# Performance work log

Hardware: AMD Instinct MI355X
Metric: run time of the kernel (lower is better)

Reference implementation:

```python
import jax, jax.numpy as jnp
import numpy as np

B, C, H, W = 4, 256, 128, 128
HEADS = 8
EPS_LN = 1e-5
EPS_NORM = 1e-12


def conv2d(x, w, padding, groups=1):
    return jax.lax.conv_general_dilated(
        x, w, window_strides=(1, 1), padding=padding,
        feature_group_count=groups,
        dimension_numbers=('NCHW', 'OIHW', 'NCHW'))


def layernorm_c(x, weight, bias):
    # WithBias LayerNorm over channel dim (to_3d makes channels the last axis)
    mu = jnp.mean(x, axis=1, keepdims=True)
    var = jnp.var(x, axis=1, keepdims=True)
    xn = (x - mu) / jnp.sqrt(var + EPS_LN)
    return xn * weight[None, :, None, None] + bias[None, :, None, None]


def setup_inputs() -> dict:
    key = jax.random.key(0)
    ks = jax.random.split(key, 8)
    s = 0.02
    return {
        'x': jax.random.normal(ks[0], (B, C, H, W), jnp.float32),
        'y': jax.random.normal(ks[1], (B, C, H, W), jnp.float32),
        'ln_kv_w': jnp.ones((C,), jnp.float32),
        'ln_kv_b': jnp.zeros((C,), jnp.float32),
        'ln_q_w': jnp.ones((C,), jnp.float32),
        'ln_q_b': jnp.zeros((C,), jnp.float32),
        'W_kv': jax.random.normal(ks[2], (2 * C, C, 1, 1), jnp.float32) * s,
        'W_dw': jax.random.normal(ks[3], (2 * C, 1, 3, 3), jnp.float32) * s,
        'W_q': jax.random.normal(ks[4], (C, C, 3, 3), jnp.float32) * s,
        'W_proj': jax.random.normal(ks[5], (C, C, 1, 1), jnp.float32) * s,
        'temperature': jnp.ones((HEADS, 1, 1), jnp.float32),
    }


def reference(x, y, ln_kv_w, ln_kv_b, ln_q_w, ln_q_b, W_kv, W_dw, W_q, W_proj, temperature):
    b, c, h, w = x.shape
    xn = layernorm_c(x, ln_kv_w, ln_kv_b)
    yn = layernorm_c(y, ln_q_w, ln_q_b)

    # Attention (MDTA channel cross-attention)
    kv = conv2d(xn, W_kv, 'VALID')                       # [b, 2c, h, w]
    kv = conv2d(kv, W_dw, 'SAME', groups=2 * c)          # depthwise 3x3
    k, v = jnp.split(kv, 2, axis=1)
    q = conv2d(yn, W_q, 'SAME')                          # [b, c, h, w]

    def heads(t):
        return t.reshape(b, HEADS, c // HEADS, h * w)    # [b, head, ch, hw]

    q, k, v = heads(q), heads(k), heads(v)
    q = q / jnp.maximum(jnp.linalg.norm(q, axis=-1, keepdims=True), EPS_NORM)
    k = k / jnp.maximum(jnp.linalg.norm(k, axis=-1, keepdims=True), EPS_NORM)

    attn = jnp.einsum('bhcn,bhdn->bhcd', q, k) * temperature[None]
    attn = jax.nn.softmax(attn, axis=-1)
    out = jnp.einsum('bhcd,bhdn->bhcn', attn, v)         # [b, head, ch, hw]
    out = out.reshape(b, c, h, w)
    out = conv2d(out, W_proj, 'VALID')
    return yn + out
```

## Files before the change

kernel.cpp:

```cpp
#include <hip/hip_runtime.h>
#include <hip/hip_bf16.h>

typedef __hip_bfloat16 bf16;
typedef __attribute__((ext_vector_type(8))) short bf16x8;
typedef __attribute__((ext_vector_type(4))) float f32x4;

#define Bn 4
#define Cn 256
#define C2n 512
#define Hn 128
#define Wn 128
#define HWn 16384
#define HEADSn 8
#define CHn 32
#define PADW 132
#define PADH 130
#define PROW (PADW * Cn)
#define PBn ((size_t)PADH * PROW)

static __device__ __forceinline__ float b2f(bf16 v) { return __bfloat162float(v); }
static __device__ __forceinline__ bf16 f2b(float v) { return __float2bfloat16(v); }
static __device__ __forceinline__ short f2bs(float v) {
    bf16 t = f2b(v);
    return __builtin_bit_cast(short, t);
}
static __device__ __forceinline__ float s2f(short s) {
    bf16 t = __builtin_bit_cast(bf16, s);
    return b2f(t);
}

static __device__ __forceinline__ void gload16(const void* g, void* l) {
    __builtin_amdgcn_global_load_lds(
        (const __attribute__((address_space(1))) unsigned int*)g,
        (__attribute__((address_space(3))) unsigned int*)l,
        16, 0, 0);
}


__global__ void cast_kernel(const float* __restrict__ src, bf16* __restrict__ dst, int n) {
    for (int i = blockIdx.x * 256 + threadIdx.x; i < n; i += gridDim.x * 256)
        dst[i] = f2b(src[i]);
}

__global__ void wq_repack_kernel(const float* __restrict__ Wq, bf16* __restrict__ wr) {
    int i = blockIdx.x * 256 + threadIdx.x;
    if (i < Cn * Cn) {
        int oc = i >> 8, c = i & 255;
        #pragma unroll
        for (int dy = 0; dy < 3; dy++)
            #pragma unroll
            for (int dx = 0; dx < 3; dx++)
                wr[((size_t)dy * Cn + oc) * 768 + dx * Cn + c] =
                    f2b(Wq[(size_t)i * 9 + dy * 3 + dx]);
    }
}

__global__ void halo_zero_kernel(bf16* __restrict__ yp) {
    int yq = blockIdx.x;
    int b  = blockIdx.y;
    bf16* row = yp + (size_t)b * PBn + (size_t)yq * PROW;
    bf16x8 z = {0, 0, 0, 0, 0, 0, 0, 0};
    if (yq == 0 || yq == PADH - 1) {
        for (int i = threadIdx.x; i < PROW / 8; i += 256)
            *(bf16x8*)&row[(size_t)i * 8] = z;
    } else {
        for (int i = threadIdx.x; i < 128; i += 256) {
            if (i < 32) *(bf16x8*)&row[(size_t)i * 8] = z;
            else        *(bf16x8*)&row[(size_t)129 * Cn + (size_t)(i - 32) * 8] = z;
        }
    }
}

__global__ void ln_kernel(const float* __restrict__ x,
                          const float* __restrict__ gw,
                          const float* __restrict__ gb,
                          bf16* __restrict__ o16) {
    __shared__ float sw[Cn], sb[Cn];
    int tid = threadIdx.x;
    if (tid < Cn) { sw[tid] = gw[tid]; sb[tid] = gb[tid]; }
    __syncthreads();
    int pix = blockIdx.x * 256 + tid;
    int b = pix >> 14;
    int hw = pix & (HWn - 1);
    const float* xb = x + (size_t)b * Cn * HWn + hw;
    float s = 0.f, ss = 0.f;
    for (int c = 0; c < Cn; c++) {
        float v = xb[(size_t)c * HWn];
        s += v; ss += v * v;
    }
    float mu  = s * (1.f / Cn);
    float var = ss * (1.f / Cn) - mu * mu;
    float inv = rsqrtf(var + 1e-5f);
    bf16* ob = o16 + (size_t)b * Cn * HWn + hw;
    for (int c = 0; c < Cn; c++) {
        float v = (xb[(size_t)c * HWn] - mu) * inv * sw[c] + sb[c];
        ob[(size_t)c * HWn] = f2b(v);
    }
}

__global__ void transpose_kernel(const bf16* __restrict__ src, bf16* __restrict__ dst) {
    __shared__ unsigned int t[64][65];
    int tid = threadIdx.x;
    int pxt = blockIdx.x;
    int ct  = blockIdx.y;
    int b   = blockIdx.z;
    const bf16* sb = src + ((size_t)b * Cn + ct * 64) * HWn + pxt * 64;
    for (int i = tid; i < 512; i += 256) {
        int r = i >> 3, sg = (i & 7) * 8;
        bf16x8 v = *(const bf16x8*)&sb[(size_t)r * HWn + sg];
        #pragma unroll
        for (int j = 0; j < 8; j++) t[r][sg + j] = (unsigned int)(unsigned short)v[j];
    }
    __syncthreads();
    bf16* db = dst + ((size_t)b * HWn + pxt * 64) * Cn + ct * 64;
    for (int i = tid; i < 512; i += 256) {
        int r = i >> 3, sg = (i & 7) * 8;
        bf16x8 v;
        #pragma unroll
        for (int j = 0; j < 8; j++) v[j] = (short)(unsigned short)t[sg + j][r];
        *(bf16x8*)&db[(size_t)r * Cn + sg] = v;
    }
}

__global__ void transpose_pad_kernel(const bf16* __restrict__ src, bf16* __restrict__ dst) {
    __shared__ unsigned int t[64][65];
    int tid = threadIdx.x;
    int pxt = blockIdx.x;
    int ct  = blockIdx.y;
    int b   = blockIdx.z;
    const bf16* sb = src + ((size_t)b * Cn + ct * 64) * HWn + pxt * 64;
    for (int i = tid; i < 512; i += 256) {
        int r = i >> 3, sg = (i & 7) * 8;
        bf16x8 v = *(const bf16x8*)&sb[(size_t)r * HWn + sg];
        #pragma unroll
        for (int j = 0; j < 8; j++) t[r][sg + j] = (unsigned int)(unsigned short)v[j];
    }
    __syncthreads();
    int p0 = pxt * 64;
    int yr = p0 >> 7, x0 = p0 & 127;
    bf16* db = dst + (size_t)b * PBn
                   + ((size_t)(yr + 1) * PADW + (x0 + 1)) * Cn + ct * 64;
    for (int i = tid; i < 512; i += 256) {
        int r = i >> 3, sg = (i & 7) * 8;
        bf16x8 v;
        #pragma unroll
        for (int j = 0; j < 8; j++) v[j] = (short)(unsigned short)t[sg + j][r];
        *(bf16x8*)&db[(size_t)r * Cn + sg] = v;
    }
}

__global__ __launch_bounds__(256) void kv1x1_mfma_kernel(
        const bf16* __restrict__ xn_pm,
        const bf16* __restrict__ wkv_pk,
        bf16* __restrict__ kv) {
    __shared__ __attribute__((aligned(16))) short Als[8192];
    __shared__ __attribute__((aligned(16))) short Bls[8192];
    int tid  = threadIdx.x;
    int px0  = blockIdx.x * 128;
    int oc0  = blockIdx.y * 128;
    int b    = blockIdx.z;
    int wave = tid >> 6, lane = tid & 63;
    int lm = lane & 15, kq = lane >> 4;
    int l7 = lm & 7;

    f32x4 acc[2][8];
    #pragma unroll
    for (int mt = 0; mt < 2; mt++)
        #pragma unroll
        for (int nt = 0; nt < 8; nt++) acc[mt][nt] = (f32x4){0.f, 0.f, 0.f, 0.f};

    int rA = tid >> 3;
    int cA = (tid & 7) ^ (rA & 7);
    const short* pA = (const short*)wkv_pk + ((size_t)(oc0 + rA)) * Cn + cA * 8;
    const short* pB = (const short*)xn_pm + ((size_t)b * HWn + px0 + rA) * Cn + cA * 8;
    short* lA = &Als[wave * 512];
    short* lB = &Bls[wave * 512];

    for (int kc = 0; kc < Cn; kc += 64) {
        __syncthreads();
        #pragma unroll
        for (int j = 0; j < 4; j++) {
            gload16(pA + kc + j * (32 * Cn), lA + j * 2048);
            gload16(pB + kc + j * (32 * Cn), lB + j * 2048);
        }
        __syncthreads();
        #pragma unroll
        for (int kk = 0; kk < 2; kk++) {
            int xo = (((kk << 2) | kq) ^ l7) * 8;
            bf16x8 afr[2], bfr[8];
            #pragma unroll
            for (int mt = 0; mt < 2; mt++)
                afr[mt] = *(const bf16x8*)&Als[(wave * 32 + mt * 16 + lm) * 64 + xo];
            #pragma unroll
            for (int nt = 0; nt < 8; nt++)
                bfr[nt] = *(const bf16x8*)&Bls[(nt * 16 + lm) * 64 + xo];
            #pragma unroll
            for (int mt = 0; mt < 2; mt++)
                #pragma unroll
                for (int nt = 0; nt < 8; nt++)
                    acc[mt][nt] = __builtin_amdgcn_mfma_f32_16x16x32_bf16(
                        afr[mt], bfr[nt], acc[mt][nt], 0, 0, 0);
        }
    }
    bf16* kb = kv + ((size_t)b * C2n + oc0) * HWn + px0;
    #pragma unroll
    for (int mt = 0; mt < 2; mt++) {
        int ocl = wave * 32 + mt * 16 + kq * 4;
        #pragma unroll
        for (int nt = 0; nt < 8; nt++) {
            int pxx = nt * 16 + lm;
            #pragma unroll
            for (int r = 0; r < 4; r++)
                kb[(size_t)(ocl + r) * HWn + pxx] = f2b(acc[mt][nt][r]);
        }
    }
}

__global__ void dw_kernel(const bf16* __restrict__ kv,
                          const float* __restrict__ Wdw,
                          bf16* __restrict__ kvdw) {
    __shared__ float st[18][132];
    int tid = threadIdx.x;
    int r0  = blockIdx.x * 16;
    int ch  = blockIdx.y;
    int b   = blockIdx.z;
    float w[9];
    #pragma unroll
    for (int t = 0; t < 9; t++) w[t] = Wdw[ch * 9 + t];
    const bf16* base = kv + ((size_t)b * C2n + ch) * HWn;
    if (tid < 18) { st[tid][0] = 0.f; st[tid][129] = 0.f; }
    for (int i = tid; i < 288; i += 256) {
        int row = i >> 4, sg = (i & 15) << 3;
        int gr = r0 - 1 + row;
        bf16x8 v = {0, 0, 0, 0, 0, 0, 0, 0};
        if (gr >= 0 && gr < Hn) v = *(const bf16x8*)&base[(size_t)gr * Wn + sg];
        #pragma unroll
        for (int j = 0; j < 8; j++) st[row][1 + sg + j] = s2f(v[j]);
    }
    __syncthreads();
    int orow = tid >> 4, sg = (tid & 15) << 3;
    float o[8];
    #pragma unroll
    for (int j = 0; j < 8; j++) o[j] = 0.f;
    #pragma unroll
    for (int dy = 0; dy < 3; dy++)
        #pragma unroll
        for (int dx = 0; dx < 3; dx++) {
            float ww = w[dy * 3 + dx];
            #pragma unroll
            for (int j = 0; j < 8; j++) o[j] += ww * st[orow + dy][sg + j + dx];
        }
    bf16x8 ov;
    #pragma unroll
    for (int j = 0; j < 8; j++) ov[j] = f2bs(o[j]);
    *(bf16x8*)&kvdw[((size_t)b * C2n + ch) * HWn + (size_t)(r0 + orow) * Wn + sg] = ov;
}

__global__ __launch_bounds__(256) void qconv_mfma_kernel(
        const bf16* __restrict__ ypad,
        const bf16* __restrict__ wq_r,
        bf16* __restrict__ q) {
    __shared__ __attribute__((aligned(16))) short Als[8192];
    __shared__ __attribute__((aligned(16))) short Bls[8192];
    int tid  = threadIdx.x;
    int xb_  = blockIdx.x;
    int y    = ((xb_ & 7) << 4) | (xb_ >> 3);
    int oc0  = blockIdx.y * 128;
    int b    = blockIdx.z;
    int wave = tid >> 6, lane = tid & 63;
    int lm = lane & 15, kq = lane >> 4;
    int l7 = lm & 7;

    f32x4 acc[2][8];
    #pragma unroll
    for (int mt = 0; mt < 2; mt++)
        #pragma unroll
        for (int nt = 0; nt < 8; nt++) acc[mt][nt] = (f32x4){0.f, 0.f, 0.f, 0.f};

    int rA = tid >> 3;
    int cA = (tid & 7) ^ (rA & 7);
    const short* pA = (const short*)wq_r + ((size_t)(oc0 + rA)) * 768 + cA * 8;
    const short* pB = (const short*)ypad + (size_t)b * PBn + (size_t)y * PROW
                    + (size_t)rA * Cn + cA * 8;
    short* lA = &Als[wave * 512];
    short* lB = &Bls[wave * 512];

    for (int dy = 0; dy < 3; dy++) {
        const short* wd = pA + (size_t)dy * (Cn * 768);
        const short* yd = pB + (size_t)dy * PROW;
        for (int kc = 0; kc < 768; kc += 64) {
            __syncthreads();
            #pragma unroll
            for (int j = 0; j < 4; j++) {
                gload16(wd + kc + j * (32 * 768), lA + j * 2048);
                gload16(yd + kc + j * (32 * Cn), lB + j * 2048);
            }
            __syncthreads();
            #pragma unroll
            for (int kk = 0; kk < 2; kk++) {
                int xo = (((kk << 2) | kq) ^ l7) * 8;
                bf16x8 afr[2], bfr[8];
                #pragma unroll
                for (int mt = 0; mt < 2; mt++)
                    afr[mt] = *(const bf16x8*)&Als[(wave * 32 + mt * 16 + lm) * 64 + xo];
                #pragma unroll
                for (int nt = 0; nt < 8; nt++)
                    bfr[nt] = *(const bf16x8*)&Bls[(nt * 16 + lm) * 64 + xo];
                #pragma unroll
                for (int mt = 0; mt < 2; mt++)
                    #pragma unroll
                    for (int nt = 0; nt < 8; nt++)
                        acc[mt][nt] = __builtin_amdgcn_mfma_f32_16x16x32_bf16(
                            afr[mt], bfr[nt], acc[mt][nt], 0, 0, 0);
            }
        }
    }
    bf16* qb = q + ((size_t)b * Cn + oc0) * HWn + (size_t)y * Wn;
    #pragma unroll
    for (int mt = 0; mt < 2; mt++) {
        int ocl = wave * 32 + mt * 16 + kq * 4;
        #pragma unroll
        for (int nt = 0; nt < 8; nt++) {
            int px = nt * 16 + lm;
            #pragma unroll
            for (int r = 0; r < 4; r++)
                qb[(size_t)(ocl + r) * HWn + px] = f2b(acc[mt][nt][r]);
        }
    }
}

__global__ __launch_bounds__(256) void attn_qk_kernel(
        const bf16* __restrict__ q,
        const bf16* __restrict__ kvdw,
        float* __restrict__ partial,
        float* __restrict__ qkp) {
    __shared__ short qls[32 * 264];
    __shared__ short kls[32 * 264];
    __shared__ float sred[4][1024];
    int tid   = threadIdx.x;
    int split = blockIdx.x;
    int bh    = blockIdx.y;
    int b = bh >> 3, h = bh & 7;
    int wave = tid >> 6, lane = tid & 63;
    int lm = lane & 15, kq = lane >> 4;

    const short* qbase = (const short*)(q    + ((size_t)(b * Cn  + h * CHn)) * HWn) + split * 2048;
    const short* kbase = (const short*)(kvdw + ((size_t)(b * C2n + h * CHn)) * HWn) + split * 2048;

    f32x4 acc[2][2];
    #pragma unroll
    for (int mt = 0; mt < 2; mt++)
        #pragma unroll
        for (int nt = 0; nt < 2; nt++) acc[mt][nt] = (f32x4){0.f, 0.f, 0.f, 0.f};

    float qss[4] = {0.f, 0.f, 0.f, 0.f};
    float kss[4] = {0.f, 0.f, 0.f, 0.f};
    int rb = tid >> 5, sgc = (tid & 31) * 8;

    for (int n0 = 0; n0 < 2048; n0 += 256) {
        __syncthreads();
        #pragma unroll
        for (int j = 0; j < 4; j++) {
            int r = rb + j * 8;
            bf16x8 qv = *(const bf16x8*)&qbase[(size_t)r * HWn + n0 + sgc];
            bf16x8 kv = *(const bf16x8*)&kbase[(size_t)r * HWn + n0 + sgc];
            *(bf16x8*)&qls[r * 264 + sgc] = qv;
            *(bf16x8*)&kls[r * 264 + sgc] = kv;
            #pragma unroll
            for (int e = 0; e < 8; e++) {
                float qf = s2f(qv[e]), kf = s2f(kv[e]);
                qss[j] += qf * qf;
                kss[j] += kf * kf;
            }
        }
        __syncthreads();
        int nb = wave * 64;
        #pragma unroll
        for (int kk = 0; kk < 64; kk += 32) {
            bf16x8 afr[2], bfr[2];
            #pragma unroll
            for (int mt = 0; mt < 2; mt++)
                afr[mt] = *(const bf16x8*)&qls[(mt * 16 + lm) * 264 + nb + kk + kq * 8];
            #pragma unroll
            for (int nt = 0; nt < 2; nt++)
                bfr[nt] = *(const bf16x8*)&kls[(nt * 16 + lm) * 264 + nb + kk + kq * 8];
            #pragma unroll
            for (int mt = 0; mt < 2; mt++)
                #pragma unroll
                for (int nt = 0; nt < 2; nt++)
                    acc[mt][nt] = __builtin_amdgcn_mfma_f32_16x16x32_bf16(
                        afr[mt], bfr[nt], acc[mt][nt], 0, 0, 0);
        }
    }
    __syncthreads();
    #pragma unroll
    for (int mt = 0; mt < 2; mt++)
        #pragma unroll
        for (int nt = 0; nt < 2; nt++)
            #pragma unroll
            for (int r = 0; r < 4; r++) {
                int c = mt * 16 + kq * 4 + r;
                int d = nt * 16 + lm;
                sred[wave][c * 32 + d] = acc[mt][nt][r];
            }
    #pragma unroll
    for (int off = 16; off > 0; off >>= 1) {
        #pragma unroll
        for (int j = 0; j < 4; j++) {
            qss[j] += __shfl_xor(qss[j], off);
            kss[j] += __shfl_xor(kss[j], off);
        }
    }
    if ((tid & 31) == 0) {
        float* qp = qkp + ((size_t)bh * 8 + split) * 64;
        #pragma unroll
        for (int j = 0; j < 4; j++) {
            qp[rb + 8 * j]      = qss[j];
            qp[32 + rb + 8 * j] = kss[j];
        }
    }
    __syncthreads();
    float* pb = partial + ((size_t)bh * 8 + split) * 1024;
    for (int i = tid; i < 1024; i += 256)
        pb[i] = sred[0][i] + sred[1][i] + sred[2][i] + sred[3][i];
}

__global__ void attn_softmax_kernel(const float* __restrict__ partial,
                                    const float* __restrict__ qkp,
                                    const float* __restrict__ temp,
                                    float* __restrict__ attn) {
    __shared__ float S[1024];
    __shared__ float sc[64];
    int bh = blockIdx.x;
    int h = bh & 7;
    int tid = threadIdx.x;
    if (tid < 64) {
        float s = 0.f;
        #pragma unroll
        for (int sp = 0; sp < 8; sp++)
            s += qkp[((size_t)bh * 8 + sp) * 64 + tid];
        sc[tid] = 1.f / fmaxf(sqrtf(s), 1e-12f);
    }
    __syncthreads();
    for (int i = tid; i < 1024; i += 256) {
        float v = 0.f;
        #pragma unroll
        for (int sp = 0; sp < 8; sp++)
            v += partial[((size_t)bh * 8 + sp) * 1024 + i];
        int c = i >> 5, d = i & 31;
        v *= sc[c] * sc[32 + d] * temp[h];
        S[i] = v;
    }
    __syncthreads();
    if (tid < 32) {
        int c = tid;
        float m = -1e30f;
        for (int d = 0; d < 32; d++) m = fmaxf(m, S[c * 32 + d]);
        float sum = 0.f;
        for (int d = 0; d < 32; d++) sum += __expf(S[c * 32 + d] - m);
        float inv = 1.f / sum;
        for (int d = 0; d < 32; d++)
            attn[(size_t)bh * 1024 + c * 32 + d] = __expf(S[c * 32 + d] - m) * inv;
    }
}

__global__ void av_kernel(const float* __restrict__ attn,
                          const bf16* __restrict__ kvdw,
                          bf16* __restrict__ ao_pm) {
    int bh = blockIdx.y;
    int b = bh >> 3, h = bh & 7;
    int tid = threadIdx.x;
    int n = blockIdx.x * 256 + tid;
    __shared__ float At[32][32];
    for (int i = tid; i < 1024; i += 256) {
        int cc = i >> 5, dd = i & 31;
        At[dd][cc] = attn[((size_t)bh * 32 + cc) * 32 + dd];
    }
    __syncthreads();
    const bf16* vbase = kvdw + ((size_t)b * C2n + Cn + h * CHn) * HWn;
    float acc[32];
    #pragma unroll
    for (int c = 0; c < 32; c++) acc[c] = 0.f;
    for (int d = 0; d < 32; d++) {
        float vv = b2f(vbase[(size_t)d * HWn + n]);
        #pragma unroll
        for (int c = 0; c < 32; c++) acc[c] += At[d][c] * vv;
    }
    bf16* obase = ao_pm + ((size_t)b * HWn + n) * Cn + h * CHn;
    #pragma unroll
    for (int g = 0; g < 4; g++) {
        bf16x8 v;
        #pragma unroll
        for (int j = 0; j < 8; j++) v[j] = f2bs(acc[g * 8 + j]);
        *(bf16x8*)&obase[g * 8] = v;
    }
}

__global__ __launch_bounds__(256) void proj_mfma_kernel(
        const bf16* __restrict__ ao_pm,
        const bf16* __restrict__ wpr_pk,
        const bf16* __restrict__ ypad,
        float* __restrict__ out) {
    __shared__ __attribute__((aligned(16))) short Als[8192];
    __shared__ __attribute__((aligned(16))) short Bls[8192];
    int tid  = threadIdx.x;
    int y    = blockIdx.x;
    int px0  = y * 128;
    int oc0  = blockIdx.y * 128;
    int b    = blockIdx.z;
    int wave = tid >> 6, lane = tid & 63;
    int lm = lane & 15, kq = lane >> 4;
    int l7 = lm & 7;

    f32x4 acc[2][8];
    #pragma unroll
    for (int mt = 0; mt < 2; mt++)
        #pragma unroll
        for (int nt = 0; nt < 8; nt++) acc[mt][nt] = (f32x4){0.f, 0.f, 0.f, 0.f};

    int rA = tid >> 3;
    int cA = (tid & 7) ^ (rA & 7);
    const short* pA = (const short*)wpr_pk + ((size_t)(oc0 + rA)) * Cn + cA * 8;
    const short* pB = (const short*)ao_pm + ((size_t)b * HWn + px0 + rA) * Cn + cA * 8;
    short* lA = &Als[wave * 512];
    short* lB = &Bls[wave * 512];

    for (int kc = 0; kc < Cn; kc += 64) {
        __syncthreads();
        #pragma unroll
        for (int j = 0; j < 4; j++) {
            gload16(pA + kc + j * (32 * Cn), lA + j * 2048);
            gload16(pB + kc + j * (32 * Cn), lB + j * 2048);
        }
        __syncthreads();
        #pragma unroll
        for (int kk = 0; kk < 2; kk++) {
            int xo = (((kk << 2) | kq) ^ l7) * 8;
            bf16x8 afr[2], bfr[8];
            #pragma unroll
            for (int mt = 0; mt < 2; mt++)
                afr[mt] = *(const bf16x8*)&Als[(wave * 32 + mt * 16 + lm) * 64 + xo];
            #pragma unroll
            for (int nt = 0; nt < 8; nt++)
                bfr[nt] = *(const bf16x8*)&Bls[(nt * 16 + lm) * 64 + xo];
            #pragma unroll
            for (int mt = 0; mt < 2; mt++)
                #pragma unroll
                for (int nt = 0; nt < 8; nt++)
                    acc[mt][nt] = __builtin_amdgcn_mfma_f32_16x16x32_bf16(
                        afr[mt], bfr[nt], acc[mt][nt], 0, 0, 0);
        }
    }
    const short* ynp = (const short*)ypad + (size_t)b * PBn
                     + ((size_t)(y + 1) * PADW + 1) * Cn;
    float* ob = out + ((size_t)b * Cn + oc0) * HWn + px0;
    #pragma unroll
    for (int mt = 0; mt < 2; mt++) {
        int ocl = wave * 32 + mt * 16 + kq * 4;
        #pragma unroll
        for (int nt = 0; nt < 8; nt++) {
            int px = nt * 16 + lm;
            #pragma unroll
            for (int r = 0; r < 4; r++)
                ob[(size_t)(ocl + r) * HWn + px] =
                    acc[mt][nt][r] + s2f(ynp[(size_t)px * Cn + oc0 + ocl + r]);
        }
    }
}

extern "C" void kernel_launch(void* const* d_in, const int* in_sizes, int n_in,
                              void* d_out, int out_size, void* d_ws, size_t ws_size,
                              hipStream_t stream) {
    const float* x     = (const float*)d_in[0];
    const float* y     = (const float*)d_in[1];
    const float* lnkw  = (const float*)d_in[2];
    const float* lnkb  = (const float*)d_in[3];
    const float* lnqw  = (const float*)d_in[4];
    const float* lnqb  = (const float*)d_in[5];
    const float* Wkv   = (const float*)d_in[6];
    const float* Wdw   = (const float*)d_in[7];
    const float* Wq    = (const float*)d_in[8];
    const float* Wproj = (const float*)d_in[9];
    const float* temp  = (const float*)d_in[10];
    float* out = (float*)d_out;

    char* ws = (char*)d_ws;
    const size_t TENB = (size_t)Bn * Cn * HWn * 2;
    bf16* xn_cm = (bf16*)ws;
    bf16* kvb   = (bf16*)ws;
    bf16* q_cm  = (bf16*)ws;
    bf16* yn_cm = (bf16*)(ws + 2 * TENB);
    bf16* kvdw  = (bf16*)(ws + 2 * TENB);
    bf16*  xn_pm = (bf16*)(ws + 4 * TENB);
    bf16*  ao_pm = xn_pm;
    float* partS = (float*)(ws + 4 * TENB);
    bf16* yn_pad = (bf16*)(ws + 5 * TENB);
    char* wp = ws + 5 * TENB + (size_t)Bn * PBn * 2;
    bf16* wq_r   = (bf16*)wp;  wp += (size_t)3 * Cn * 768 * 2;
    bf16* wkv_pk = (bf16*)wp;  wp += (size_t)C2n * Cn * 2;
    bf16* wpr_pk = (bf16*)wp;  wp += (size_t)Cn * Cn * 2;
    float* qkp   = (float*)wp; wp += 65536;
    float* attnP = (float*)wp; wp += 131072;

    wq_repack_kernel<<<dim3(256), 256, 0, stream>>>(Wq, wq_r);
    cast_kernel<<<dim3(128), 256, 0, stream>>>(Wkv, wkv_pk, C2n * Cn);
    cast_kernel<<<dim3(64), 256, 0, stream>>>(Wproj, wpr_pk, Cn * Cn);
    halo_zero_kernel<<<dim3(PADH, Bn), 256, 0, stream>>>(yn_pad);
    ln_kernel<<<dim3(Bn * HWn / 256), 256, 0, stream>>>(x, lnkw, lnkb, xn_cm);
    ln_kernel<<<dim3(Bn * HWn / 256), 256, 0, stream>>>(y, lnqw, lnqb, yn_cm);
    transpose_kernel<<<dim3(HWn / 64, Cn / 64, Bn), 256, 0, stream>>>(xn_cm, xn_pm);
    transpose_pad_kernel<<<dim3(HWn / 64, Cn / 64, Bn), 256, 0, stream>>>(yn_cm, yn_pad);
    kv1x1_mfma_kernel<<<dim3(HWn / 128, C2n / 128, Bn), 256, 0, stream>>>(xn_pm, wkv_pk, kvb);
    dw_kernel<<<dim3(Hn / 16, C2n, Bn), 256, 0, stream>>>(kvb, Wdw, kvdw);
    qconv_mfma_kernel<<<dim3(Hn, Cn / 128, Bn), 256, 0, stream>>>(yn_pad, wq_r, q_cm);
    attn_qk_kernel<<<dim3(8, Bn * HEADSn), 256, 0, stream>>>(q_cm, kvdw, partS, qkp);
    attn_softmax_kernel<<<dim3(Bn * HEADSn), 256, 0, stream>>>(partS, qkp, temp, attnP);
    av_kernel<<<dim3(HWn / 256, Bn * HEADSn), 256, 0, stream>>>(attnP, kvdw, ao_pm);
    proj_mfma_kernel<<<dim3(HWn / 128, Cn / 128, Bn), 256, 0, stream>>>(ao_pm, wpr_pk, yn_pad, out);
}
```

Measured before the change: 489.0 us.

## Fuse layernorm apply into transpose and double-buffer qconv LDS pipeline

Result: faster. 470.9 us (-3.7%).

```diff
diff --git a/kernel.cpp b/kernel.cpp
--- a/kernel.cpp
+++ b/kernel.cpp
@@ -71,18 +71,15 @@
     }
 }
 
-__global__ void ln_kernel(const float* __restrict__ x,
-                          const float* __restrict__ gw,
-                          const float* __restrict__ gb,
-                          bf16* __restrict__ o16) {
-    __shared__ float sw[Cn], sb[Cn];
-    int tid = threadIdx.x;
-    if (tid < Cn) { sw[tid] = gw[tid]; sb[tid] = gb[tid]; }
-    __syncthreads();
-    int pix = blockIdx.x * 256 + tid;
+__global__ void ln_stats_kernel(const float* __restrict__ x,
+                                const float* __restrict__ y,
+                                float* __restrict__ stats) {
+    int which = blockIdx.y;
+    const float* src = which ? y : x;
+    int pix = blockIdx.x * 256 + threadIdx.x;
     int b = pix >> 14;
     int hw = pix & (HWn - 1);
-    const float* xb = x + (size_t)b * Cn * HWn + hw;
+    const float* xb = src + (size_t)b * Cn * HWn + hw;
     float s = 0.f, ss = 0.f;
     for (int c = 0; c < Cn; c++) {
         float v = xb[(size_t)c * HWn];
@@ -91,61 +88,50 @@
     float mu  = s * (1.f / Cn);
     float var = ss * (1.f / Cn) - mu * mu;
     float inv = rsqrtf(var + 1e-5f);
-    bf16* ob = o16 + (size_t)b * Cn * HWn + hw;
-    for (int c = 0; c < Cn; c++) {
-        float v = (xb[(size_t)c * HWn] - mu) * inv * sw[c] + sb[c];
-        ob[(size_t)c * HWn] = f2b(v);
-    }
-}
-
-__global__ void transpose_kernel(const bf16* __restrict__ src, bf16* __restrict__ dst) {
-    __shared__ unsigned int t[64][65];
+    float* st = stats + (size_t)which * 2 * Bn * HWn;
+    st[pix] = mu;
+    st[(size_t)Bn * HWn + pix] = inv;
+}
+
+__global__ void transpose_ln_kernel(const float* __restrict__ src,
+                                    const float* __restrict__ stats,
+                                    const float* __restrict__ gw,
+                                    const float* __restrict__ gb,
+                                    bf16* __restrict__ dst, int pad) {
+    __shared__ float t[64][65];
+    __shared__ float swv[64], sbv[64], smu[64], sinv[64];
     int tid = threadIdx.x;
     int pxt = blockIdx.x;
     int ct  = blockIdx.y;
     int b   = blockIdx.z;
-    const bf16* sb = src + ((size_t)b * Cn + ct * 64) * HWn + pxt * 64;
+    int p0  = pxt * 64;
+    if (tid < 64)       { swv[tid] = gw[ct * 64 + tid]; sbv[tid] = gb[ct * 64 + tid]; }
+    else if (tid < 128) { int p = tid - 64;  smu[p]  = stats[(size_t)b * HWn + p0 + p]; }
+    else if (tid < 192) { int p = tid - 128; sinv[p] = stats[(size_t)Bn * HWn + (size_t)b * HWn + p0 + p]; }
+    const float* sb_ = src + ((size_t)b * Cn + ct * 64) * HWn + p0;
+    for (int i = tid; i < 1024; i += 256) {
+        int r = i >> 4, sg = (i & 15) * 4;
+        float4 v = *(const float4*)&sb_[(size_t)r * HWn + sg];
+        t[r][sg + 0] = v.x; t[r][sg + 1] = v.y; t[r][sg + 2] = v.z; t[r][sg + 3] = v.w;
+    }
+    __syncthreads();
+    size_t base;
+    if (pad) {
+        int yr = p0 >> 7, x0 = p0 & 127;
+        base = (size_t)b * PBn + ((size_t)(yr + 1) * PADW + (x0 + 1)) * Cn + ct * 64;
+    } else {
+        base = ((size_t)b * HWn + p0) * Cn + ct * 64;
+    }
     for (int i = tid; i < 512; i += 256) {
-        int r = i >> 3, sg = (i & 7) * 8;
-        bf16x8 v = *(const bf16x8*)&sb[(size_t)r * HWn + sg];
-        #pragma unroll
-        for (int j = 0; j < 8; j++) t[r][sg + j] = (unsigned int)(unsigned short)v[j];
-    }
-    __syncthreads();
-    bf16* db = dst + ((size_t)b * HWn + pxt * 64) * Cn + ct * 64;
-    for (int i = tid; i < 512; i += 256) {
-        int r = i >> 3, sg = (i & 7) * 8;
+        int p = i >> 3, cg = (i & 7) * 8;
+        float mu = smu[p], inv = sinv[p];
         bf16x8 v;
         #pragma unroll
-        for (int j = 0; j < 8; j++) v[j] = (short)(unsigned short)t[sg + j][r];
-        *(bf16x8*)&db[(size_t)r * Cn + sg] = v;
-    }
-}
-
-__global__ void transpose_pad_kernel(const bf16* __restrict__ src, bf16* __restrict__ dst) {
-    __shared__ unsigned int t[64][65];
-    int tid = threadIdx.x;
-    int pxt = blockIdx.x;
-    int ct  = blockIdx.y;
-    int b   = blockIdx.z;
-    const bf16* sb = src + ((size_t)b * Cn + ct * 64) * HWn + pxt * 64;
-    for (int i = tid; i < 512; i += 256) {
-        int r = i >> 3, sg = (i & 7) * 8;
-        bf16x8 v = *(const bf16x8*)&sb[(size_t)r * HWn + sg];
-        #pragma unroll
-        for (int j = 0; j < 8; j++) t[r][sg + j] = (unsigned int)(unsigned short)v[j];
-    }
-    __syncthreads();
-    int p0 = pxt * 64;
-    int yr = p0 >> 7, x0 = p0 & 127;
-    bf16* db = dst + (size_t)b * PBn
-                   + ((size_t)(yr + 1) * PADW + (x0 + 1)) * Cn + ct * 64;
-    for (int i = tid; i < 512; i += 256) {
-        int r = i >> 3, sg = (i & 7) * 8;
-        bf16x8 v;
-        #pragma unroll
-        for (int j = 0; j < 8; j++) v[j] = (short)(unsigned short)t[sg + j][r];
-        *(bf16x8*)&db[(size_t)r * Cn + sg] = v;
+        for (int j = 0; j < 8; j++) {
+            float val = (t[cg + j][p] - mu) * inv * swv[cg + j] + sbv[cg + j];
+            v[j] = f2bs(val);
+        }
+        *(bf16x8*)&dst[base + (size_t)p * Cn + cg] = v;
     }
 }
 
@@ -256,12 +242,12 @@
     *(bf16x8*)&kvdw[((size_t)b * C2n + ch) * HWn + (size_t)(r0 + orow) * Wn + sg] = ov;
 }
 
-__global__ __launch_bounds__(256) void qconv_mfma_kernel(
+__global__ __launch_bounds__(256, 2) void qconv_mfma_kernel(
         const bf16* __restrict__ ypad,
         const bf16* __restrict__ wq_r,
         bf16* __restrict__ q) {
-    __shared__ __attribute__((aligned(16))) short Als[8192];
-    __shared__ __attribute__((aligned(16))) short Bls[8192];
+    __shared__ __attribute__((aligned(16))) short Als[2][8192];
+    __shared__ __attribute__((aligned(16))) short Bls[2][8192];
     int tid  = threadIdx.x;
     int xb_  = blockIdx.x;
     int y    = ((xb_ & 7) << 4) | (xb_ >> 3);
@@ -279,42 +265,60 @@
 
     int rA = tid >> 3;
     int cA = (tid & 7) ^ (rA & 7);
-    const short* pA = (const short*)wq_r + ((size_t)(oc0 + rA)) * 768 + cA * 8;
-    const short* pB = (const short*)ypad + (size_t)b * PBn + (size_t)y * PROW
-                    + (size_t)rA * Cn + cA * 8;
-    short* lA = &Als[wave * 512];
-    short* lB = &Bls[wave * 512];
-
-    for (int dy = 0; dy < 3; dy++) {
-        const short* wd = pA + (size_t)dy * (Cn * 768);
-        const short* yd = pB + (size_t)dy * PROW;
-        for (int kc = 0; kc < 768; kc += 64) {
-            __syncthreads();
-            #pragma unroll
-            for (int j = 0; j < 4; j++) {
-                gload16(wd + kc + j * (32 * 768), lA + j * 2048);
-                gload16(yd + kc + j * (32 * Cn), lB + j * 2048);
-            }
-            __syncthreads();
-            #pragma unroll
-            for (int kk = 0; kk < 2; kk++) {
-                int xo = (((kk << 2) | kq) ^ l7) * 8;
-                bf16x8 afr[2], bfr[8];
-                #pragma unroll
-                for (int mt = 0; mt < 2; mt++)
-                    afr[mt] = *(const bf16x8*)&Als[(wave * 32 + mt * 16 + lm) * 64 + xo];
+    const short* pwA = (const short*)wq_r + ((size_t)(oc0 + rA)) * 768 + cA * 8;
+    const short* pwB = (const short*)ypad + (size_t)b * PBn + (size_t)y * PROW
+                     + (size_t)rA * Cn + cA * 8;
+    int pk = 0;
+
+#define STGQ(sel) { \
+    short* la_ = &Als[sel][wave * 512]; \
+    short* lb_ = &Bls[sel][wave * 512]; \
+    _Pragma("unroll") \
+    for (int j = 0; j < 4; j++) { \
+        gload16(pwA + j * (32 * 768), la_ + j * 2048); \
+        gload16(pwB + j * (32 * Cn),  lb_ + j * 2048); } }
+#define BUMPQ() { \
+    pk++; pwA += 64; pwB += 64; \
+    if (pk == 12) { pk = 0; pwA += Cn * 768 - 768; pwB += PROW - 768; } }
+
+    STGQ(0); BUMPQ();
+    STGQ(1); BUMPQ();
+    asm volatile("s_waitcnt vmcnt(8)" ::: "memory");
+    __builtin_amdgcn_s_barrier();
+
+    for (int t = 0; t < 36; t++) {
+        int cur = t & 1;
+        const short* Ab = &Als[cur][0];
+        const short* Bb = &Bls[cur][0];
+        bf16x8 afr[2][2], bfr[2][8];
+        #pragma unroll
+        for (int kk = 0; kk < 2; kk++) {
+            int xo = (((kk << 2) | kq) ^ l7) * 8;
+            #pragma unroll
+            for (int mt = 0; mt < 2; mt++)
+                afr[kk][mt] = *(const bf16x8*)&Ab[(wave * 32 + mt * 16 + lm) * 64 + xo];
+            #pragma unroll
+            for (int nt = 0; nt < 8; nt++)
+                bfr[kk][nt] = *(const bf16x8*)&Bb[(nt * 16 + lm) * 64 + xo];
+        }
+        asm volatile("s_waitcnt lgkmcnt(0)" ::: "memory");
+        __builtin_amdgcn_sched_barrier(0);
+        __builtin_amdgcn_s_barrier();
+        if (t < 34) { STGQ(cur); BUMPQ(); }
+        #pragma unroll
+        for (int kk = 0; kk < 2; kk++)
+            #pragma unroll
+            for (int mt = 0; mt < 2; mt++)
                 #pragma unroll
                 for (int nt = 0; nt < 8; nt++)
-                    bfr[nt] = *(const bf16x8*)&Bls[(nt * 16 + lm) * 64 + xo];
-                #pragma unroll
-                for (int mt = 0; mt < 2; mt++)
-                    #pragma unroll
-                    for (int nt = 0; nt < 8; nt++)
-                        acc[mt][nt] = __builtin_amdgcn_mfma_f32_16x16x32_bf16(
-                            afr[mt], bfr[nt], acc[mt][nt], 0, 0, 0);
-            }
-        }
-    }
+                    acc[mt][nt] = __builtin_amdgcn_mfma_f32_16x16x32_bf16(
+                        afr[kk][mt], bfr[kk][nt], acc[mt][nt], 0, 0, 0);
+        if (t < 34) asm volatile("s_waitcnt vmcnt(8)" ::: "memory");
+        else        asm volatile("s_waitcnt vmcnt(0)" ::: "memory");
+        __builtin_amdgcn_s_barrier();
+    }
+#undef STGQ
+#undef BUMPQ
     bf16* qb = q + ((size_t)b * Cn + oc0) * HWn + (size_t)y * Wn;
     #pragma unroll
     for (int mt = 0; mt < 2; mt++) {
@@ -586,10 +590,8 @@
 
     char* ws = (char*)d_ws;
     const size_t TENB = (size_t)Bn * Cn * HWn * 2;
-    bf16* xn_cm = (bf16*)ws;
     bf16* kvb   = (bf16*)ws;
     bf16* q_cm  = (bf16*)ws;
-    bf16* yn_cm = (bf16*)(ws + 2 * TENB);
     bf16* kvdw  = (bf16*)(ws + 2 * TENB);
     bf16*  xn_pm = (bf16*)(ws + 4 * TENB);
     bf16*  ao_pm = xn_pm;
@@ -601,15 +603,17 @@
     bf16* wpr_pk = (bf16*)wp;  wp += (size_t)Cn * Cn * 2;
     float* qkp   = (float*)wp; wp += 65536;
     float* attnP = (float*)wp; wp += 131072;
+    float* stats = (float*)wp; wp += (size_t)2 * 2 * Bn * HWn * 4;
 
     wq_repack_kernel<<<dim3(256), 256, 0, stream>>>(Wq, wq_r);
     cast_kernel<<<dim3(128), 256, 0, stream>>>(Wkv, wkv_pk, C2n * Cn);
     cast_kernel<<<dim3(64), 256, 0, stream>>>(Wproj, wpr_pk, Cn * Cn);
     halo_zero_kernel<<<dim3(PADH, Bn), 256, 0, stream>>>(yn_pad);
-    ln_kernel<<<dim3(Bn * HWn / 256), 256, 0, stream>>>(x, lnkw, lnkb, xn_cm);
-    ln_kernel<<<dim3(Bn * HWn / 256), 256, 0, stream>>>(y, lnqw, lnqb, yn_cm);
-    transpose_kernel<<<dim3(HWn / 64, Cn / 64, Bn), 256, 0, stream>>>(xn_cm, xn_pm);
-    transpose_pad_kernel<<<dim3(HWn / 64, Cn / 64, Bn), 256, 0, stream>>>(yn_cm, yn_pad);
+    ln_stats_kernel<<<dim3(Bn * HWn / 256, 2), 256, 0, stream>>>(x, y, stats);
+    transpose_ln_kernel<<<dim3(HWn / 64, Cn / 64, Bn), 256, 0, stream>>>(
+        x, stats, lnkw, lnkb, xn_pm, 0);
+    transpose_ln_kernel<<<dim3(HWn / 64, Cn / 64, Bn), 256, 0, stream>>>(
+        y, stats + (size_t)2 * Bn * HWn, lnqw, lnqb, yn_pad, 1);
     kv1x1_mfma_kernel<<<dim3(HWn / 128, C2n / 128, Bn), 256, 0, stream>>>(xn_pm, wkv_pk, kvb);
     dw_kernel<<<dim3(Hn / 16, C2n, Bn), 256, 0, stream>>>(kvb, Wdw, kvdw);
     qconv_mfma_kernel<<<dim3(Hn, Cn / 128, Bn), 256, 0, stream>>>(yn_pad, wq_r, q_cm);
```
